# Performance work log

Measured on AMD Instinct MI355X. Metric: run time of the kernel, lower is better.

The kernel has to match this reference:

```python
import jax, jax.numpy as jnp
import numpy as np

# hyperparameters (match init_kwargs)
V_TH = 0.4
V_RESET = 0.0
LEAK = 0.01
REFR_LEAK = 0.01
REFR_POT = 0.0
STD_POT = 0.0
REFRAC = 2.0
ALPHA = 20.0

IN_FEATURES = 1024
OUT_CLASSES = 512
BATCH = 128
T_STEPS = 256


@jax.custom_vjp
def spike_fn(x):
    return (x > 0.0).astype(x.dtype)

def _spike_fwd(x):
    return spike_fn(x), x

def _spike_bwd(x, g):
    denom = 1.0 + jnp.abs(ALPHA * x)
    return (g * (ALPHA / (denom * denom)),)

spike_fn.defvjp(_spike_fwd, _spike_bwd)


def _snn_forward(x_seq, W):
    B = x_seq.shape[0]
    C = W.shape[1]
    V0 = jnp.zeros((B, C), jnp.float32)
    refr0 = jnp.zeros((B, C), jnp.float32)
    mode0 = jnp.zeros((B, C), jnp.int32)
    sc0 = jnp.zeros((B, C), jnp.float32)

    def step(carry, x_t):
        V, refr, mode, sc = carry
        I_t = x_t @ W  # [B,C]
        m_std = mode == 0
        m_abs = mode == 1
        m_rel = mode == 2
        # --- standard mode: integrate, leak, floor, spike ---
        V = jnp.where(m_std, V + I_t - LEAK, V)
        V = jnp.where(m_std & (V < STD_POT), STD_POT, V)
        s = spike_fn(V - V_TH) * m_std.astype(jnp.float32)
        fired = s > 0.0
        sc = sc + s
        V = jnp.where(fired, V_RESET, V)
        refr = jnp.where(fired, REFRAC, refr)
        mode = jnp.where(fired, 1, mode)
        # --- absolute refractory: count down ---
        refr = jnp.where(m_abs, jnp.maximum(refr - 1.0, 0.0), refr)
        done = m_abs & (refr <= 0.0)
        mode = jnp.where(done, 2, mode)
        V = jnp.where(m_abs & (V < REFR_POT), REFR_POT, V)
        # --- relative refractory: recover toward standard ---
        V = jnp.where(m_rel, V + REFR_LEAK, V)
        V = jnp.where(m_rel & (V < REFR_POT), REFR_POT, V)
        back = m_rel & (V > STD_POT)
        mode = jnp.where(back, 0, mode)
        return (V, refr, mode, sc), None

    xs = jnp.transpose(x_seq, (1, 0, 2))  # [T,B,F]
    (_, _, _, spike_counts), _ = jax.lax.scan(step, (V0, refr0, mode0, sc0), xs)
    return spike_counts


def setup_inputs() -> dict:
    key = jax.random.key(0)
    k1, k2 = jax.random.split(key)
    x_seq = jax.random.uniform(k1, (BATCH, T_STEPS, IN_FEATURES), dtype=jnp.float32)
    # HeNormal initializer: std = sqrt(2 / fan_in)
    W = jax.random.normal(k2, (IN_FEATURES, OUT_CLASSES), dtype=jnp.float32) * np.sqrt(2.0 / IN_FEATURES)
    return {"x_seq": x_seq, "W": W}


def reference(x_seq, W):
    return _snn_forward(x_seq, W)
```

## Files before the change

kernel.cpp:

```cpp
#include <hip/hip_runtime.h>

#define B_ 128
#define T_ 256
#define F_ 1024
#define C_ 512
#define K_ F_

typedef _Float16 f16;
typedef f16 f16x8 __attribute__((ext_vector_type(8)));
typedef f16 f16x4 __attribute__((ext_vector_type(4)));
typedef float f32x4 __attribute__((ext_vector_type(4)));

__global__ __launch_bounds__(256) void wsplit_kernel(
    const float* __restrict__ W, f16* __restrict__ WhiT,
    f16* __restrict__ WloT) {
  __shared__ float tile[32][33];
  const int k0 = blockIdx.x * 32;
  const int n0 = blockIdx.y * 32;
  const int tid = threadIdx.x;
#pragma unroll
  for (int j = 0; j < 4; ++j) {
    const int e = tid + 256 * j;
    const int r = e >> 5, c = e & 31;
    tile[r][c] = W[(size_t)(k0 + r) * C_ + n0 + c];
  }
  __syncthreads();
#pragma unroll
  for (int j = 0; j < 4; ++j) {
    const int e = tid + 256 * j;
    const int nn = e >> 5, kk = e & 31;
    const float w = tile[kk][nn];
    const f16 wh = (f16)w;
    const f16 wl = (f16)((w - (float)wh) * 4096.0f);
    WhiT[(size_t)(n0 + nn) * K_ + k0 + kk] = wh;
    WloT[(size_t)(n0 + nn) * K_ + k0 + kk] = wl;
  }
}

__global__ __launch_bounds__(256) void xsplit_kernel(
    const float* __restrict__ X, f16* __restrict__ Ahi, f16* __restrict__ Alo,
    int t0, int lct, int total4) {
  const int ctm1 = (1 << lct) - 1;
  for (int i4 = blockIdx.x * 256 + threadIdx.x; i4 < total4;
       i4 += gridDim.x * 256) {
    const int m = i4 >> 8;
    const int f4 = (i4 & 255) * 4;
    const int xrow = (m >> lct) * T_ + t0 + (m & ctm1);
    const float4 v = *(const float4*)(X + (size_t)xrow * F_ + f4);
    const f16 h0 = (f16)v.x, h1 = (f16)v.y, h2 = (f16)v.z, h3 = (f16)v.w;
    const f16 l0 = (f16)((v.x - (float)h0) * 4096.0f);
    const f16 l1 = (f16)((v.y - (float)h1) * 4096.0f);
    const f16 l2 = (f16)((v.z - (float)h2) * 4096.0f);
    const f16 l3 = (f16)((v.w - (float)h3) * 4096.0f);
    f16x4 hv = {h0, h1, h2, h3};
    f16x4 lv = {l0, l1, l2, l3};
    *(f16x4*)(Ahi + (size_t)m * K_ + f4) = hv;
    *(f16x4*)(Alo + (size_t)m * K_ + f4) = lv;
  }
}

#define LDT 40

__global__ __launch_bounds__(256) void snn_gemm_mfma(
    const f16* __restrict__ Ahi, const f16* __restrict__ Alo,
    const f16* __restrict__ WhiT, const f16* __restrict__ WloT,
    float* __restrict__ I) {
  __shared__ f16 sAh[128 * LDT];
  __shared__ f16 sAl[128 * LDT];
  __shared__ f16 sBh[128 * LDT];
  __shared__ f16 sBl[128 * LDT];

  const int tid = threadIdx.x;
  const int m0 = blockIdx.x * 128;
  const int n0 = blockIdx.y * 128;
  const int lane = tid & 63;
  const int w = tid >> 6;
  const int wm = (w >> 1) * 64, wn = (w & 1) * 64;

  const int r0 = tid >> 2, s0 = (tid & 3) * 8;
  const f16* gAh0 = Ahi + (size_t)(m0 + r0) * K_ + s0;
  const f16* gAl0 = Alo + (size_t)(m0 + r0) * K_ + s0;
  const f16* gBh0 = WhiT + (size_t)(n0 + r0) * K_ + s0;
  const f16* gBl0 = WloT + (size_t)(n0 + r0) * K_ + s0;
  const size_t gstep = (size_t)64 * K_;
  const int wr0 = r0 * LDT + s0;
  const int wr1 = (r0 + 64) * LDT + s0;

  uint4 vAh0 = *(const uint4*)(gAh0);
  uint4 vAh1 = *(const uint4*)(gAh0 + gstep);
  uint4 vAl0 = *(const uint4*)(gAl0);
  uint4 vAl1 = *(const uint4*)(gAl0 + gstep);
  uint4 vBh0 = *(const uint4*)(gBh0);
  uint4 vBh1 = *(const uint4*)(gBh0 + gstep);
  uint4 vBl0 = *(const uint4*)(gBl0);
  uint4 vBl1 = *(const uint4*)(gBl0 + gstep);

  f32x4 acc0[4][4] = {};
  f32x4 acc1[4][4] = {};

  for (int kt = 0; kt < K_ / 32; ++kt) {
    __syncthreads();
    *(uint4*)&sAh[wr0] = vAh0;
    *(uint4*)&sAh[wr1] = vAh1;
    *(uint4*)&sAl[wr0] = vAl0;
    *(uint4*)&sAl[wr1] = vAl1;
    *(uint4*)&sBh[wr0] = vBh0;
    *(uint4*)&sBh[wr1] = vBh1;
    *(uint4*)&sBl[wr0] = vBl0;
    *(uint4*)&sBl[wr1] = vBl1;
    __syncthreads();
    if (kt + 1 < K_ / 32) {
      const int ko = (kt + 1) * 32;
      vAh0 = *(const uint4*)(gAh0 + ko);
      vAh1 = *(const uint4*)(gAh0 + gstep + ko);
      vAl0 = *(const uint4*)(gAl0 + ko);
      vAl1 = *(const uint4*)(gAl0 + gstep + ko);
      vBh0 = *(const uint4*)(gBh0 + ko);
      vBh1 = *(const uint4*)(gBh0 + gstep + ko);
      vBl0 = *(const uint4*)(gBl0 + ko);
      vBl1 = *(const uint4*)(gBl0 + gstep + ko);
    }
    const int lrow = lane & 15;
    const int sl = (lane >> 4) * 8;
    f16x8 Bh[4], Bl[4];
#pragma unroll
    for (int fn = 0; fn < 4; ++fn) {
      const int nrow = (wn + fn * 16 + lrow) * LDT + sl;
      Bh[fn] = *(const f16x8*)&sBh[nrow];
      Bl[fn] = *(const f16x8*)&sBl[nrow];
    }
#pragma unroll
    for (int fm = 0; fm < 4; ++fm) {
      const int mrow = (wm + fm * 16 + lrow) * LDT + sl;
      const f16x8 Ah = *(const f16x8*)&sAh[mrow];
      const f16x8 Al = *(const f16x8*)&sAl[mrow];
#pragma unroll
      for (int fn = 0; fn < 4; ++fn) {
        acc0[fm][fn] = __builtin_amdgcn_mfma_f32_16x16x32_f16(
            Ah, Bh[fn], acc0[fm][fn], 0, 0, 0);
        acc1[fm][fn] = __builtin_amdgcn_mfma_f32_16x16x32_f16(
            Al, Bh[fn], acc1[fm][fn], 0, 0, 0);
        acc1[fm][fn] = __builtin_amdgcn_mfma_f32_16x16x32_f16(
            Ah, Bl[fn], acc1[fm][fn], 0, 0, 0);
      }
    }
  }

  const int er = (lane >> 4) * 4;
  const int ec = lane & 15;
#pragma unroll
  for (int fm = 0; fm < 4; ++fm)
#pragma unroll
    for (int fn = 0; fn < 4; ++fn) {
      float* op =
          I + (size_t)(m0 + wm + fm * 16 + er) * C_ + n0 + wn + fn * 16 + ec;
#pragma unroll
      for (int i = 0; i < 4; ++i)
        op[(size_t)i * C_] = acc0[fm][fn][i] + acc1[fm][fn][i] * (1.0f / 4096.0f);
    }
}

#define GRP 32

#define STEP(Iv)                                                           \
  {                                                                        \
    const bool is0 = (mode == 0), is1 = (mode == 1), is2 = (mode == 2);    \
    V = is0 ? ((V + (Iv)) - 0.01f) : (is2 ? (V + 0.01f) : V);              \
    V = fmaxf(V, 0.0f);                                                    \
    const bool fired = is0 && ((V - 0.4f) > 0.0f);                         \
    sc += fired ? 1.0f : 0.0f;                                             \
    refr = fired ? 2.0f : (is1 ? fmaxf(refr - 1.0f, 0.0f) : refr);         \
    const bool done = is1 && (refr <= 0.0f);                               \
    const bool back = is2 && (V > 0.0f);                                   \
    V = fired ? 0.0f : V;                                                  \
    mode = fired ? 1 : (done ? 2 : (back ? 0 : mode));                     \
  }

__global__ __launch_bounds__(256) void snn_scan_kernel(
    const float* __restrict__ I, float* __restrict__ Vst,
    float* __restrict__ Rst, int* __restrict__ Mst, float* __restrict__ SCst,
    float* __restrict__ out, int CT, int first, int last) {
  const int idx = blockIdx.x * 256 + threadIdx.x;
  float V, refr, sc;
  int mode;
  if (first) {
    V = 0.f; refr = 0.f; sc = 0.f; mode = 0;
  } else {
    V = Vst[idx]; refr = Rst[idx]; mode = Mst[idx]; sc = SCst[idx];
  }
  const int b = idx >> 9;
  const int c = idx & 511;
  const float* Ip = I + (size_t)b * CT * C_ + c;

  float bufA[GRP], bufB[GRP];
  const int ng = CT / GRP;

#pragma unroll
  for (int j = 0; j < GRP; ++j) bufA[j] = Ip[(size_t)j * C_];

  for (int g = 0; g < ng; g += 2) {
    if (g + 1 < ng) {
      const float* p = Ip + (size_t)(g + 1) * GRP * C_;
#pragma unroll
      for (int j = 0; j < GRP; ++j) bufB[j] = p[(size_t)j * C_];
    }
#pragma unroll
    for (int j = 0; j < GRP; ++j) STEP(bufA[j]);
    if (g + 1 < ng) {
      if (g + 2 < ng) {
        const float* p = Ip + (size_t)(g + 2) * GRP * C_;
#pragma unroll
        for (int j = 0; j < GRP; ++j) bufA[j] = p[(size_t)j * C_];
      }
#pragma unroll
      for (int j = 0; j < GRP; ++j) STEP(bufB[j]);
    }
  }

  if (last) {
    out[idx] = sc;
  } else {
    Vst[idx] = V; Rst[idx] = refr; Mst[idx] = mode; SCst[idx] = sc;
  }
}

extern "C" void kernel_launch(void* const* d_in, const int* in_sizes, int n_in,
                              void* d_out, int out_size, void* d_ws,
                              size_t ws_size, hipStream_t stream) {
  const float* X = (const float*)d_in[0];
  const float* Wm = (const float*)d_in[1];
  float* out = (float*)d_out;

  int CT = 256, lct = 8;
  while (CT > 16) {
    const size_t need = (size_t)B_ * CT * C_ * 4
                        + (size_t)2 * B_ * CT * K_ * 2
                        + (size_t)2 * C_ * K_ * 2
                        + (size_t)4 * B_ * C_ * 4;
    if (need <= ws_size) break;
    CT >>= 1;
    --lct;
  }

  char* p = (char*)d_ws;
  float* Ibuf = (float*)p; p += (size_t)B_ * CT * C_ * 4;
  f16* Ahi = (f16*)p; p += (size_t)B_ * CT * K_ * 2;
  f16* Alo = (f16*)p; p += (size_t)B_ * CT * K_ * 2;
  f16* WhiT = (f16*)p; p += (size_t)C_ * K_ * 2;
  f16* WloT = (f16*)p; p += (size_t)C_ * K_ * 2;
  float* Vst = (float*)p;
  float* Rst = Vst + B_ * C_;
  float* SCst = Rst + B_ * C_;
  int* Mst = (int*)(SCst + B_ * C_);

  wsplit_kernel<<<dim3(K_ / 32, C_ / 32), 256, 0, stream>>>(Wm, WhiT, WloT);

  const int total4 = B_ * CT * (K_ / 4);
  const dim3 ggrid(B_ * CT / 128, C_ / 128);
  for (int t0 = 0; t0 < T_; t0 += CT) {
    xsplit_kernel<<<2048, 256, 0, stream>>>(X, Ahi, Alo, t0, lct, total4);
    snn_gemm_mfma<<<ggrid, 256, 0, stream>>>(Ahi, Alo, WhiT, WloT, Ibuf);
    snn_scan_kernel<<<(B_ * C_) / 256, 256, 0, stream>>>(
        Ibuf, Vst, Rst, Mst, SCst, out, CT, t0 == 0, (t0 + CT) == T_);
  }
}
```

Baseline: 364.9 us.

## Fuse fp16 hi/lo split of X into GEMM and stage scan inputs through LDS

Drops the separate xsplit kernel: the GEMM now loads fp32 X directly and splits it into hi/lo fp16 in registers after the MFMA loop, so the Ahi/Alo buffers are never written to or read back from global memory. The time-chunking loop and the state save/restore between chunks are removed, so all T steps run as one GEMM and one scan launch. The scan kernel now loads coalesced 64-step tiles into shared memory with float4 loads instead of doing strided per-thread loads. The GEMM carries more live registers and reads twice the A bytes as fp32, and the workspace size check is gone, so it now assumes the full I buffer fits.

```diff
diff --git a/kernel.cpp b/kernel.cpp
--- a/kernel.cpp
+++ b/kernel.cpp
@@ -8,7 +8,6 @@
 
 typedef _Float16 f16;
 typedef f16 f16x8 __attribute__((ext_vector_type(8)));
-typedef f16 f16x4 __attribute__((ext_vector_type(4)));
 typedef float f32x4 __attribute__((ext_vector_type(4)));
 
 __global__ __launch_bounds__(256) void wsplit_kernel(
@@ -37,34 +36,11 @@
   }
 }
 
-__global__ __launch_bounds__(256) void xsplit_kernel(
-    const float* __restrict__ X, f16* __restrict__ Ahi, f16* __restrict__ Alo,
-    int t0, int lct, int total4) {
-  const int ctm1 = (1 << lct) - 1;
-  for (int i4 = blockIdx.x * 256 + threadIdx.x; i4 < total4;
-       i4 += gridDim.x * 256) {
-    const int m = i4 >> 8;
-    const int f4 = (i4 & 255) * 4;
-    const int xrow = (m >> lct) * T_ + t0 + (m & ctm1);
-    const float4 v = *(const float4*)(X + (size_t)xrow * F_ + f4);
-    const f16 h0 = (f16)v.x, h1 = (f16)v.y, h2 = (f16)v.z, h3 = (f16)v.w;
-    const f16 l0 = (f16)((v.x - (float)h0) * 4096.0f);
-    const f16 l1 = (f16)((v.y - (float)h1) * 4096.0f);
-    const f16 l2 = (f16)((v.z - (float)h2) * 4096.0f);
-    const f16 l3 = (f16)((v.w - (float)h3) * 4096.0f);
-    f16x4 hv = {h0, h1, h2, h3};
-    f16x4 lv = {l0, l1, l2, l3};
-    *(f16x4*)(Ahi + (size_t)m * K_ + f4) = hv;
-    *(f16x4*)(Alo + (size_t)m * K_ + f4) = lv;
-  }
-}
-
 #define LDT 40
 
 __global__ __launch_bounds__(256) void snn_gemm_mfma(
-    const f16* __restrict__ Ahi, const f16* __restrict__ Alo,
-    const f16* __restrict__ WhiT, const f16* __restrict__ WloT,
-    float* __restrict__ I) {
+    const float* __restrict__ X, const f16* __restrict__ WhiT,
+    const f16* __restrict__ WloT, float* __restrict__ I) {
   __shared__ f16 sAh[128 * LDT];
   __shared__ f16 sAl[128 * LDT];
   __shared__ f16 sBh[128 * LDT];
@@ -78,47 +54,65 @@
   const int wm = (w >> 1) * 64, wn = (w & 1) * 64;
 
   const int r0 = tid >> 2, s0 = (tid & 3) * 8;
-  const f16* gAh0 = Ahi + (size_t)(m0 + r0) * K_ + s0;
-  const f16* gAl0 = Alo + (size_t)(m0 + r0) * K_ + s0;
+  const float* gA0 = X + (size_t)(m0 + r0) * K_ + s0;
+  const float* gA1 = X + (size_t)(m0 + r0 + 64) * K_ + s0;
   const f16* gBh0 = WhiT + (size_t)(n0 + r0) * K_ + s0;
   const f16* gBl0 = WloT + (size_t)(n0 + r0) * K_ + s0;
-  const size_t gstep = (size_t)64 * K_;
+  const size_t gstepB = (size_t)64 * K_;
   const int wr0 = r0 * LDT + s0;
   const int wr1 = (r0 + 64) * LDT + s0;
 
-  uint4 vAh0 = *(const uint4*)(gAh0);
-  uint4 vAh1 = *(const uint4*)(gAh0 + gstep);
-  uint4 vAl0 = *(const uint4*)(gAl0);
-  uint4 vAl1 = *(const uint4*)(gAl0 + gstep);
-  uint4 vBh0 = *(const uint4*)(gBh0);
-  uint4 vBh1 = *(const uint4*)(gBh0 + gstep);
-  uint4 vBl0 = *(const uint4*)(gBl0);
-  uint4 vBl1 = *(const uint4*)(gBl0 + gstep);
+  float4 xa0, xa1, xb0, xb1;
+  uint4 vBh0, vBh1, vBl0, vBl1;
+  f16x8 Ah0, Al0, Ah1, Al1;
+
+#define SPLIT8(p0, p1, H, L)                                   \
+  {                                                            \
+    const float v_[8] = {(p0).x, (p0).y, (p0).z, (p0).w,       \
+                         (p1).x, (p1).y, (p1).z, (p1).w};      \
+    _Pragma("unroll") for (int j_ = 0; j_ < 8; ++j_) {         \
+      const f16 h_ = (f16)v_[j_];                              \
+      (H)[j_] = h_;                                            \
+      (L)[j_] = (f16)((v_[j_] - (float)h_) * 4096.0f);         \
+    }                                                          \
+  }
+
+  xa0 = *(const float4*)(gA0);
+  xa1 = *(const float4*)(gA0 + 4);
+  xb0 = *(const float4*)(gA1);
+  xb1 = *(const float4*)(gA1 + 4);
+  vBh0 = *(const uint4*)(gBh0);
+  vBh1 = *(const uint4*)(gBh0 + gstepB);
+  vBl0 = *(const uint4*)(gBl0);
+  vBl1 = *(const uint4*)(gBl0 + gstepB);
+  SPLIT8(xa0, xa1, Ah0, Al0);
+  SPLIT8(xb0, xb1, Ah1, Al1);
 
   f32x4 acc0[4][4] = {};
   f32x4 acc1[4][4] = {};
 
   for (int kt = 0; kt < K_ / 32; ++kt) {
     __syncthreads();
-    *(uint4*)&sAh[wr0] = vAh0;
-    *(uint4*)&sAh[wr1] = vAh1;
-    *(uint4*)&sAl[wr0] = vAl0;
-    *(uint4*)&sAl[wr1] = vAl1;
+    *(f16x8*)&sAh[wr0] = Ah0;
+    *(f16x8*)&sAh[wr1] = Ah1;
+    *(f16x8*)&sAl[wr0] = Al0;
+    *(f16x8*)&sAl[wr1] = Al1;
     *(uint4*)&sBh[wr0] = vBh0;
     *(uint4*)&sBh[wr1] = vBh1;
     *(uint4*)&sBl[wr0] = vBl0;
     *(uint4*)&sBl[wr1] = vBl1;
     __syncthreads();
-    if (kt + 1 < K_ / 32) {
+    const bool more = (kt + 1 < K_ / 32);
+    if (more) {
       const int ko = (kt + 1) * 32;
-      vAh0 = *(const uint4*)(gAh0 + ko);
-      vAh1 = *(const uint4*)(gAh0 + gstep + ko);
-      vAl0 = *(const uint4*)(gAl0 + ko);
-      vAl1 = *(const uint4*)(gAl0 + gstep + ko);
+      xa0 = *(const float4*)(gA0 + ko);
+      xa1 = *(const float4*)(gA0 + ko + 4);
+      xb0 = *(const float4*)(gA1 + ko);
+      xb1 = *(const float4*)(gA1 + ko + 4);
       vBh0 = *(const uint4*)(gBh0 + ko);
-      vBh1 = *(const uint4*)(gBh0 + gstep + ko);
+      vBh1 = *(const uint4*)(gBh0 + gstepB + ko);
       vBl0 = *(const uint4*)(gBl0 + ko);
-      vBl1 = *(const uint4*)(gBl0 + gstep + ko);
+      vBl1 = *(const uint4*)(gBl0 + gstepB + ko);
     }
     const int lrow = lane & 15;
     const int sl = (lane >> 4) * 8;
@@ -144,6 +138,10 @@
             Ah, Bl[fn], acc1[fm][fn], 0, 0, 0);
       }
     }
+    if (more) {
+      SPLIT8(xa0, xa1, Ah0, Al0);
+      SPLIT8(xb0, xb1, Ah1, Al1);
+    }
   }
 
   const int er = (lane >> 4) * 4;
@@ -160,7 +158,7 @@
     }
 }
 
-#define GRP 32
+#define TT 64
 
 #define STEP(Iv)                                                           \
   {                                                                        \
@@ -177,51 +175,39 @@
   }
 
 __global__ __launch_bounds__(256) void snn_scan_kernel(
-    const float* __restrict__ I, float* __restrict__ Vst,
-    float* __restrict__ Rst, int* __restrict__ Mst, float* __restrict__ SCst,
-    float* __restrict__ out, int CT, int first, int last) {
-  const int idx = blockIdx.x * 256 + threadIdx.x;
-  float V, refr, sc;
-  int mode;
-  if (first) {
-    V = 0.f; refr = 0.f; sc = 0.f; mode = 0;
-  } else {
-    V = Vst[idx]; refr = Rst[idx]; mode = Mst[idx]; sc = SCst[idx];
-  }
-  const int b = idx >> 9;
-  const int c = idx & 511;
-  const float* Ip = I + (size_t)b * CT * C_ + c;
-
-  float bufA[GRP], bufB[GRP];
-  const int ng = CT / GRP;
-
-#pragma unroll
-  for (int j = 0; j < GRP; ++j) bufA[j] = Ip[(size_t)j * C_];
-
-  for (int g = 0; g < ng; g += 2) {
-    if (g + 1 < ng) {
-      const float* p = Ip + (size_t)(g + 1) * GRP * C_;
-#pragma unroll
-      for (int j = 0; j < GRP; ++j) bufB[j] = p[(size_t)j * C_];
-    }
-#pragma unroll
-    for (int j = 0; j < GRP; ++j) STEP(bufA[j]);
-    if (g + 1 < ng) {
-      if (g + 2 < ng) {
-        const float* p = Ip + (size_t)(g + 2) * GRP * C_;
-#pragma unroll
-        for (int j = 0; j < GRP; ++j) bufA[j] = p[(size_t)j * C_];
-      }
-#pragma unroll
-      for (int j = 0; j < GRP; ++j) STEP(bufB[j]);
-    }
-  }
-
-  if (last) {
-    out[idx] = sc;
-  } else {
-    Vst[idx] = V; Rst[idx] = refr; Mst[idx] = mode; SCst[idx] = sc;
-  }
+    const float* __restrict__ I, float* __restrict__ out) {
+  __shared__ float tile[TT * 256];
+  const int tid = threadIdx.x;
+  const int bid = blockIdx.x;
+  const int b = bid >> 1;
+  const int c0 = (bid & 1) << 8;
+  const float* Ib = I + (size_t)b * T_ * C_ + c0;
+
+  float V = 0.f, refr = 0.f, sc = 0.f;
+  int mode = 0;
+
+  for (int tg = 0; tg < T_ / TT; ++tg) {
+    float4 st[16];
+#pragma unroll
+    for (int i = 0; i < 16; ++i) {
+      const int flat4 = i * 256 + tid;
+      const int row = flat4 >> 6, col4 = flat4 & 63;
+      st[i] = *(const float4*)(Ib + (size_t)(tg * TT + row) * C_ + col4 * 4);
+    }
+    __syncthreads();
+#pragma unroll
+    for (int i = 0; i < 16; ++i) {
+      const int flat4 = i * 256 + tid;
+      *(float4*)&tile[flat4 * 4] = st[i];
+    }
+    __syncthreads();
+#pragma unroll
+    for (int tt = 0; tt < TT; ++tt) {
+      const float Iv = tile[tt * 256 + tid];
+      STEP(Iv);
+    }
+  }
+  out[bid * 256 + tid] = sc;
 }
 
 extern "C" void kernel_launch(void* const* d_in, const int* in_sizes, int n_in,
@@ -231,36 +217,13 @@
   const float* Wm = (const float*)d_in[1];
   float* out = (float*)d_out;
 
-  int CT = 256, lct = 8;
-  while (CT > 16) {
-    const size_t need = (size_t)B_ * CT * C_ * 4
-                        + (size_t)2 * B_ * CT * K_ * 2
-                        + (size_t)2 * C_ * K_ * 2
-                        + (size_t)4 * B_ * C_ * 4;
-    if (need <= ws_size) break;
-    CT >>= 1;
-    --lct;
-  }
-
   char* p = (char*)d_ws;
-  float* Ibuf = (float*)p; p += (size_t)B_ * CT * C_ * 4;
-  f16* Ahi = (f16*)p; p += (size_t)B_ * CT * K_ * 2;
-  f16* Alo = (f16*)p; p += (size_t)B_ * CT * K_ * 2;
-  f16* WhiT = (f16*)p; p += (size_t)C_ * K_ * 2;
-  f16* WloT = (f16*)p; p += (size_t)C_ * K_ * 2;
-  float* Vst = (float*)p;
-  float* Rst = Vst + B_ * C_;
-  float* SCst = Rst + B_ * C_;
-  int* Mst = (int*)(SCst + B_ * C_);
+  float* Ibuf = (float*)p; p += (size_t)B_ * T_ * C_ * sizeof(float);
+  f16* WhiT = (f16*)p; p += (size_t)C_ * K_ * sizeof(f16);
+  f16* WloT = (f16*)p;
 
   wsplit_kernel<<<dim3(K_ / 32, C_ / 32), 256, 0, stream>>>(Wm, WhiT, WloT);
-
-  const int total4 = B_ * CT * (K_ / 4);
-  const dim3 ggrid(B_ * CT / 128, C_ / 128);
-  for (int t0 = 0; t0 < T_; t0 += CT) {
-    xsplit_kernel<<<2048, 256, 0, stream>>>(X, Ahi, Alo, t0, lct, total4);
-    snn_gemm_mfma<<<ggrid, 256, 0, stream>>>(Ahi, Alo, WhiT, WloT, Ibuf);
-    snn_scan_kernel<<<(B_ * C_) / 256, 256, 0, stream>>>(
-        Ibuf, Vst, Rst, Mst, SCst, out, CT, t0 == 0, (t0 + CT) == T_);
-  }
-}
+  snn_gemm_mfma<<<dim3(B_ * T_ / 128, C_ / 128), 256, 0, stream>>>(
+      X, WhiT, WloT, Ibuf);
+  snn_scan_kernel<<<B_ * C_ / 256, 256, 0, stream>>>(Ibuf, out);
+}
```

Result: faster. 339.9 us (-6.9%).
